# Kernel optimization log

Measured on AMD Instinct MI355X. Metric: run time of the kernel, lower is better.

Reference implementation:

```python
import jax, jax.numpy as jnp
import numpy as np

N, E, Q = 50000, 800000, 2000000   # nodes, edges, quadruplets
F_IN, H, OUT, G = 128, 128, 1, 64  # in_channels, hidden, out_channels, graphs
NRBF = NCBF = NSBF = 6
L = 3  # num_layers


def _mlp2(h, Wa, ba, Wb, bb):
    # Linear -> ReLU -> Linear
    return jax.nn.relu(h @ Wa + ba) @ Wb + bb


def setup_inputs() -> dict:
    key = jax.random.key(0)
    ks = jax.random.split(key, 24)
    s = 0.05
    inp = {
        "x": jax.random.normal(ks[0], (N, F_IN), jnp.float32),
        "rbf": jax.random.normal(ks[1], (E, NRBF), jnp.float32),
        "cbf": jax.random.normal(ks[2], (Q, NCBF), jnp.float32),
        "sbf": jax.random.normal(ks[3], (Q, NSBF), jnp.float32),
        "edge_index": jax.random.randint(ks[4], (2, E), 0, N),
        "l_idx": jax.random.randint(ks[5], (Q,), 0, N),
        "k_idx": jax.random.randint(ks[6], (Q,), 0, E),
        "batch": jnp.sort(jax.random.randint(ks[7], (N,), 0, G)),
        # per-layer params (all layers share shapes since F_IN == H)
        "W_e1a": s * jax.random.normal(ks[8], (L, F_IN + NRBF + NCBF + NSBF, H)),
        "b_e1a": jnp.zeros((L, H)),
        "W_e1b": s * jax.random.normal(ks[9], (L, H, H)),
        "b_e1b": jnp.zeros((L, H)),
        "W_e2a": s * jax.random.normal(ks[10], (L, 2 * H, H)),
        "b_e2a": jnp.zeros((L, H)),
        "W_e2b": s * jax.random.normal(ks[11], (L, H, H)),
        "b_e2b": jnp.zeros((L, H)),
        "W_na": s * jax.random.normal(ks[12], (L, F_IN + H, H)),
        "b_na": jnp.zeros((L, H)),
        "W_nb": s * jax.random.normal(ks[13], (L, H, H)),
        "b_nb": jnp.zeros((L, H)),
        "W_oa": s * jax.random.normal(ks[14], (H, H)),
        "b_oa": jnp.zeros((H,)),
        "W_ob": s * jax.random.normal(ks[15], (H, OUT)),
        "b_ob": jnp.zeros((OUT,)),
    }
    return inp


def reference(x, rbf, cbf, sbf,
              W_e1a, b_e1a, W_e1b, b_e1b,
              W_e2a, b_e2a, W_e2b, b_e2b,
              W_na, b_na, W_nb, b_nb,
              W_oa, b_oa, W_ob, b_ob,
              edge_index, l_idx, k_idx, batch):
    src, dst = edge_index[0], edge_index[1]  # x_j = x[src], index = dst
    h = x
    for p in range(L):
        # quadruplet message: gather-concat-MLP  [Q, F+18] -> [Q, H]
        m_in = jnp.concatenate([h[l_idx], rbf[k_idx], cbf, sbf], axis=-1)
        em = _mlp2(m_in, W_e1a[p], b_e1a[p], W_e1b[p], b_e1b[p])
        # scatter-add quadruplet messages onto edges by k_idx -> [E, H]
        agg_e = jax.ops.segment_sum(em, k_idx, num_segments=E)
        # second stage: per-edge concat (note: aggregated indexed by dst, as in source)
        fin = jnp.concatenate([h[src], agg_e[dst]], axis=-1)
        msg = _mlp2(fin, W_e2a[p], b_e2a[p], W_e2b[p], b_e2b[p])
        # aggregate edge messages to target nodes -> [N, H]
        aggr = jax.ops.segment_sum(msg, dst, num_segments=N)
        h = _mlp2(jnp.concatenate([h, aggr], axis=-1), W_na[p], b_na[p], W_nb[p], b_nb[p])
    # global mean pool over graphs
    counts = jax.ops.segment_sum(jnp.ones((N, 1), h.dtype), batch, num_segments=G)
    pooled = jax.ops.segment_sum(h, batch, num_segments=G) / jnp.maximum(counts, 1.0)
    pooled = jax.nn.relu(pooled)
    return _mlp2(pooled, W_oa, b_oa, W_ob, b_ob)
```

## Files before the change

### kernel.cpp

```cpp
#include <hip/hip_runtime.h>

constexpr int Nn = 50000;
constexpr int Ee = 800000;
constexpr int Qq = 2000000;
constexpr int Gg = 64;
constexpr int Hh = 128;
constexpr int NB64 = (Nn + 63) / 64;
constexpr int NSCB = (Nn + 1023) / 1024;

typedef short bf16x8 __attribute__((ext_vector_type(8)));
typedef float f32x4  __attribute__((ext_vector_type(4)));

__device__ __forceinline__ unsigned short f2bf(float f) {
    unsigned u = __builtin_bit_cast(unsigned, f);
    u += 0x7FFFu + ((u >> 16) & 1u);
    return (unsigned short)(u >> 16);
}
__device__ __forceinline__ float bf2f(unsigned short s) {
    unsigned u = ((unsigned)s) << 16;
    return __builtin_bit_cast(float, u);
}

__global__ void k_hist2(const int* __restrict__ dst, const int* __restrict__ kidx,
                        int* __restrict__ hist_e, int* __restrict__ hist_q) {
    int i = blockIdx.x * blockDim.x + threadIdx.x;
    if (i < Ee) atomicAdd(&hist_e[dst[i]], 1);
    if (i < Qq) { int v = kidx[i]; if (v < Nn) atomicAdd(&hist_q[v], 1); }
}

__global__ __launch_bounds__(1024) void k_scanA2(const int* __restrict__ he,
                                                 const int* __restrict__ hq,
                                                 int* __restrict__ ce, int* __restrict__ cq,
                                                 int* __restrict__ bs) {
    __shared__ int s[1024];
    const int* h = blockIdx.y ? hq : he;
    int* c = blockIdx.y ? cq : ce;
    int* b = bs + blockIdx.y * 64;
    const int tid = threadIdx.x;
    int i = blockIdx.x * 1024 + tid;
    int v = (i < Nn) ? h[i] : 0;
    s[tid] = v;
    __syncthreads();
    for (int off = 1; off < 1024; off <<= 1) {
        int t = (tid >= off) ? s[tid - off] : 0;
        __syncthreads();
        s[tid] += t;
        __syncthreads();
    }
    if (i < Nn) c[i] = s[tid] - v;
    if (tid == 1023) b[blockIdx.x] = s[1023];
}
__global__ void k_scanB2(int* __restrict__ bs) {
    __shared__ int s[64];
    int* b = bs + blockIdx.x * 64;
    const int tid = threadIdx.x;
    int v = (tid < NSCB) ? b[tid] : 0;
    s[tid] = v;
    __syncthreads();
    for (int off = 1; off < 64; off <<= 1) {
        int t = (tid >= off) ? s[tid - off] : 0;
        __syncthreads();
        s[tid] += t;
        __syncthreads();
    }
    if (tid < NSCB) b[tid] = s[tid] - v;
}
__global__ __launch_bounds__(1024) void k_scanC2(int* __restrict__ ce, int* __restrict__ cq,
                                                 const int* __restrict__ bs) {
    int* c = blockIdx.y ? cq : ce;
    const int* b = bs + blockIdx.y * 64;
    int i = blockIdx.x * 1024 + threadIdx.x;
    if (i < Nn) c[i] += b[blockIdx.x];
}

__global__ void k_scatter_both(const int* __restrict__ dst, const int* __restrict__ src,
                               const int* __restrict__ kidx, const int* __restrict__ lidx,
                               const float* __restrict__ cbf, const float* __restrict__ sbf,
                               int* __restrict__ cur_e, int* __restrict__ cur_q,
                               int* __restrict__ srcs, int* __restrict__ lq,
                               unsigned short* __restrict__ qfeat) {
    int i = blockIdx.x * blockDim.x + threadIdx.x;
    if (i < Ee) {
        int p = atomicAdd(&cur_e[dst[i]], 1);
        srcs[p] = src[i];
    }
    if (i < Qq) {
        int v = kidx[i];
        if (v < Nn) {
            int p = atomicAdd(&cur_q[v], 1);
            lq[p] = lidx[i];
            unsigned short f[12];
#pragma unroll
            for (int k = 0; k < 6; ++k) f[k] = f2bf(cbf[(size_t)i * 6 + k]);
#pragma unroll
            for (int k = 0; k < 6; ++k) f[6 + k] = f2bf(sbf[(size_t)i * 6 + k]);
            *(uint2*)&qfeat[(size_t)p * 12]     = *(uint2*)&f[0];
            *(uint2*)&qfeat[(size_t)p * 12 + 4] = *(uint2*)&f[4];
            *(uint2*)&qfeat[(size_t)p * 12 + 8] = *(uint2*)&f[8];
        }
    }
}

__global__ void k_wtall(const float* __restrict__ We1a0, const float* __restrict__ We1b0,
                        const float* __restrict__ We2a0, const float* __restrict__ We2b0,
                        const float* __restrict__ Wna0,  const float* __restrict__ Wnb0,
                        unsigned short* __restrict__ wbuf) {
    int idx = blockIdx.x * blockDim.x + threadIdx.x;
    if (idx >= 135168) return;
    const int p = blockIdx.y;
    const float* We1a = We1a0 + (size_t)p * 146 * 128;
    const float* We1b = We1b0 + (size_t)p * 128 * 128;
    const float* We2a = We2a0 + (size_t)p * 256 * 128;
    const float* We2b = We2b0 + (size_t)p * 128 * 128;
    const float* Wna  = Wna0  + (size_t)p * 256 * 128;
    const float* Wnb  = Wnb0  + (size_t)p * 128 * 128;
    unsigned short* base = wbuf + (size_t)p * 135168;
    const float* src; int K, Kp, loc;
    if (idx < 16384)       { src = We1a;             K = 128; Kp = 128; loc = idx; }
    else if (idx < 20480)  { src = We1a + 128 * 128; K = 6;   Kp = 32;  loc = idx - 16384; }
    else if (idx < 36864)  { src = We1b;             K = 128; Kp = 128; loc = idx - 20480; }
    else if (idx < 69632)  { src = We2a;             K = 256; Kp = 256; loc = idx - 36864; }
    else if (idx < 86016)  { src = We2b;             K = 128; Kp = 128; loc = idx - 69632; }
    else if (idx < 118784) { src = Wna;              K = 256; Kp = 256; loc = idx - 86016; }
    else                   { src = Wnb;              K = 128; Kp = 128; loc = idx - 118784; }
    int n = loc / Kp, k = loc - n * Kp;
    base[idx] = (k < K) ? f2bf(src[(size_t)k * 128 + n]) : (unsigned short)0;
}

__device__ __forceinline__ void zacc(f32x4 acc[4][2]) {
#pragma unroll
    for (int rt = 0; rt < 4; ++rt)
#pragma unroll
        for (int ct = 0; ct < 2; ++ct)
            acc[rt][ct] = (f32x4){0.f, 0.f, 0.f, 0.f};
}

template<int KK, int SA, int KP>
__device__ __forceinline__ void gemm64(const unsigned short* A,
                                       const unsigned short* __restrict__ Wt,
                                       int k_off, f32x4 acc[4][2]) {
    const int tid = threadIdx.x;
    const int lane = tid & 63;
    const int nb = (tid >> 6) * 32;
    const int rA = lane & 15;
    const int kg = lane >> 4;
#pragma unroll
    for (int ks = 0; ks < KK / 32; ++ks) {
        const int ka = ks * 32 + kg * 8;
        const int kb = k_off + ka;
        bf16x8 b0 = *(const bf16x8*)&Wt[(size_t)(nb + rA) * KP + kb];
        bf16x8 b1 = *(const bf16x8*)&Wt[(size_t)(nb + 16 + rA) * KP + kb];
#pragma unroll
        for (int rt = 0; rt < 4; ++rt) {
            bf16x8 a = *(const bf16x8*)&A[(rt * 16 + rA) * SA + ka];
            acc[rt][0] = __builtin_amdgcn_mfma_f32_16x16x32_bf16(a, b0, acc[rt][0], 0, 0, 0);
            acc[rt][1] = __builtin_amdgcn_mfma_f32_16x16x32_bf16(a, b1, acc[rt][1], 0, 0, 0);
        }
    }
}

__device__ __forceinline__ void store_acc(const f32x4 acc[4][2], unsigned short* out,
                                          int n0, int nmax) {
    const int tid = threadIdx.x;
    const int lane = tid & 63;
    const int nb = (tid >> 6) * 32;
    const int rA = lane & 15, kg = lane >> 4;
#pragma unroll
    for (int rt = 0; rt < 4; ++rt)
#pragma unroll
        for (int ct = 0; ct < 2; ++ct) {
            int col = nb + ct * 16 + rA;
#pragma unroll
            for (int i = 0; i < 4; ++i) {
                int n = n0 + rt * 16 + kg * 4 + i;
                if (n < nmax) out[(size_t)n * 128 + col] = f2bf(acc[rt][ct][i]);
            }
        }
}

__global__ __launch_bounds__(256) void k_pre0(
    const float* __restrict__ x, const float* __restrict__ rbf,
    const unsigned short* __restrict__ wbuf,
    unsigned short* __restrict__ hb,
    unsigned short* __restrict__ P1, unsigned short* __restrict__ Z1,
    unsigned short* __restrict__ P2all)
{
    __shared__ unsigned short TA[64 * 136];
    const int m0 = blockIdx.x * 64;
    const int tid = threadIdx.x;
    for (int i = tid; i < 64 * 32; i += 256) {
        int row = i >> 5, c = i & 31;
        int n = m0 + row;
        int nc = min(n, Nn - 1);
        float4 v = *(const float4*)&x[(size_t)nc * 128 + c * 4];
        ushort4 o;
        o.x = f2bf(v.x); o.y = f2bf(v.y); o.z = f2bf(v.z); o.w = f2bf(v.w);
        *(ushort4*)&TA[row * 136 + c * 4] = o;
        if (n < Nn) *(ushort4*)&hb[(size_t)n * 128 + c * 4] = o;
    }
    __syncthreads();
    f32x4 acc[4][2];
    zacc(acc);
    gemm64<128, 136, 128>(TA, wbuf, 0, acc);
    store_acc(acc, P1, m0, Nn);
    zacc(acc);
    gemm64<128, 136, 256>(TA, wbuf + 36864, 0, acc);
    store_acc(acc, Z1, m0, Nn);
    __syncthreads();
    for (int i = tid; i < 64 * 32; i += 256) {
        int row = i >> 5, c = i & 31;
        int nc = min(m0 + row, Nn - 1);
        float v = (c < 6) ? rbf[(size_t)nc * 6 + c] : 0.f;
        TA[row * 136 + c] = f2bf(v);
    }
    __syncthreads();
    for (int p = 0; p < 3; ++p) {
        zacc(acc);
        gemm64<32, 136, 32>(TA, wbuf + (size_t)p * 135168 + 16384, 0, acc);
        store_acc(acc, P2all + (size_t)p * Nn * 128, m0, Nn);
    }
}

__global__ __launch_bounds__(256) void k_quadagg(
    const unsigned short* __restrict__ P1, const unsigned short* __restrict__ P2,
    const unsigned short* __restrict__ qfeat, const int* __restrict__ lq,
    const int* __restrict__ rowend, const int* __restrict__ rowcnt,
    const float* __restrict__ We1a_raw, const float* __restrict__ b_e1a,
    unsigned short* __restrict__ Rb)
{
    __shared__ float W34[12 * 128];
    __shared__ float bia[128];
    const int tid = threadIdx.x;
    for (int i = tid; i < 12 * 128; i += 256) W34[i] = We1a_raw[134 * 128 + i];
    if (tid < 128) bia[tid] = b_e1a[tid];
    __syncthreads();
    const int nd = tid >> 4;
    const int c0 = (tid & 15) * 8;
    const int n = blockIdx.x * 16 + nd;
    const int end = rowend[n];
    const int beg = end - rowcnt[n];
    float base[8];
    {
        uint4 p2v = *(const uint4*)&P2[(size_t)n * 128 + c0];
        const unsigned short* pp = (const unsigned short*)&p2v;
#pragma unroll
        for (int k = 0; k < 8; ++k) base[k] = bia[c0 + k] + bf2f(pp[k]);
    }
    float acc[8];
#pragma unroll
    for (int k = 0; k < 8; ++k) acc[k] = 0.f;
    for (int e = beg; e < end; ++e) {
        int l = lq[e];
        uint4 a = *(const uint4*)&P1[(size_t)l * 128 + c0];
        uint2 f0 = *(const uint2*)&qfeat[(size_t)e * 12];
        uint2 f1 = *(const uint2*)&qfeat[(size_t)e * 12 + 4];
        uint2 f2 = *(const uint2*)&qfeat[(size_t)e * 12 + 8];
        const unsigned short* q0 = (const unsigned short*)&f0;
        const unsigned short* q1 = (const unsigned short*)&f1;
        const unsigned short* q2 = (const unsigned short*)&f2;
        float qv[12] = {bf2f(q0[0]), bf2f(q0[1]), bf2f(q0[2]), bf2f(q0[3]),
                        bf2f(q1[0]), bf2f(q1[1]), bf2f(q1[2]), bf2f(q1[3]),
                        bf2f(q2[0]), bf2f(q2[1]), bf2f(q2[2]), bf2f(q2[3])};
        const unsigned short* ap = (const unsigned short*)&a;
        float t[8];
#pragma unroll
        for (int k = 0; k < 8; ++k) t[k] = base[k] + bf2f(ap[k]);
#pragma unroll
        for (int kk = 0; kk < 12; ++kk) {
            float q_ = qv[kk];
#pragma unroll
            for (int k = 0; k < 8; ++k)
                t[k] = fmaf(q_, W34[kk * 128 + c0 + k], t[k]);
        }
#pragma unroll
        for (int k = 0; k < 8; ++k) acc[k] += fmaxf(t[k], 0.f);
    }
    unsigned short ov[8];
#pragma unroll
    for (int k = 0; k < 8; ++k) ov[k] = f2bf(acc[k]);
    *(uint4*)&Rb[(size_t)n * 128 + c0] = *(uint4*)ov;
}

__global__ __launch_bounds__(256) void k_edgeagg(
    const unsigned short* __restrict__ Z1, const unsigned short* __restrict__ Z2,
    const int* __restrict__ srcs,
    const int* __restrict__ rowend, const int* __restrict__ rowcnt,
    const float* __restrict__ b_e2a,
    unsigned short* __restrict__ Rb)
{
    const int tid = threadIdx.x;
    const int nd = tid >> 4;
    const int c0 = (tid & 15) * 8;
    const int n = blockIdx.x * 16 + nd;
    const int end = rowend[n];
    const int beg = end - rowcnt[n];
    float z2b[8];
    {
        uint4 zv = *(const uint4*)&Z2[(size_t)n * 128 + c0];
        const unsigned short* zp = (const unsigned short*)&zv;
        float4 b0 = *(const float4*)&b_e2a[c0];
        float4 b1 = *(const float4*)&b_e2a[c0 + 4];
        z2b[0] = b0.x + bf2f(zp[0]); z2b[1] = b0.y + bf2f(zp[1]);
        z2b[2] = b0.z + bf2f(zp[2]); z2b[3] = b0.w + bf2f(zp[3]);
        z2b[4] = b1.x + bf2f(zp[4]); z2b[5] = b1.y + bf2f(zp[5]);
        z2b[6] = b1.z + bf2f(zp[6]); z2b[7] = b1.w + bf2f(zp[7]);
    }
    float acc[8];
#pragma unroll
    for (int k = 0; k < 8; ++k) acc[k] = 0.f;
    int e = beg;
    for (; e + 2 <= end; e += 2) {
        int s0 = srcs[e], s1 = srcs[e + 1];
        uint4 a0 = *(const uint4*)&Z1[(size_t)s0 * 128 + c0];
        uint4 a1 = *(const uint4*)&Z1[(size_t)s1 * 128 + c0];
        const unsigned short* p0 = (const unsigned short*)&a0;
        const unsigned short* p1 = (const unsigned short*)&a1;
#pragma unroll
        for (int k = 0; k < 8; ++k) acc[k] += fmaxf(z2b[k] + bf2f(p0[k]), 0.f);
#pragma unroll
        for (int k = 0; k < 8; ++k) acc[k] += fmaxf(z2b[k] + bf2f(p1[k]), 0.f);
    }
    if (e < end) {
        int s0 = srcs[e];
        uint4 a0 = *(const uint4*)&Z1[(size_t)s0 * 128 + c0];
        const unsigned short* p0 = (const unsigned short*)&a0;
#pragma unroll
        for (int k = 0; k < 8; ++k) acc[k] += fmaxf(z2b[k] + bf2f(p0[k]), 0.f);
    }
    unsigned short ov[8];
#pragma unroll
    for (int k = 0; k < 8; ++k) ov[k] = f2bf(acc[k]);
    *(uint4*)&Rb[(size_t)n * 128 + c0] = *(uint4*)ov;
}

__global__ __launch_bounds__(256) void k_agg2z(
    const unsigned short* __restrict__ Rb, const int* __restrict__ cntq,
    const unsigned short* __restrict__ wb, const float* __restrict__ b_e1b,
    unsigned short* __restrict__ Z2)
{
    __shared__ unsigned short L[64 * 136];
    __shared__ int rc[64];
    const int m0 = blockIdx.x * 64;
    const int tid = threadIdx.x;
    const unsigned short* We1bt = wb + 20480;
    const unsigned short* We2at = wb + 36864;
    if (tid < 64) rc[tid] = (m0 + tid < Nn) ? cntq[m0 + tid] : 0;
    for (int i = tid; i < 64 * 16; i += 256) {
        int row = i >> 4, ch = i & 15;
        int n = min(m0 + row, Nn - 1);
        *(uint4*)&L[row * 136 + ch * 8] = *(const uint4*)&Rb[(size_t)n * 128 + ch * 8];
    }
    __syncthreads();
    f32x4 acc[4][2];
    zacc(acc);
    gemm64<128, 136, 128>(L, We1bt, 0, acc);
    __syncthreads();
    {
        const int lane = tid & 63;
        const int nb = (tid >> 6) * 32;
        const int rA = lane & 15, kg = lane >> 4;
#pragma unroll
        for (int rt = 0; rt < 4; ++rt)
#pragma unroll
            for (int ct = 0; ct < 2; ++ct) {
                int col = nb + ct * 16 + rA;
                float bias = b_e1b[col];
#pragma unroll
                for (int i = 0; i < 4; ++i) {
                    int row = rt * 16 + kg * 4 + i;
                    L[row * 136 + col] = f2bf(acc[rt][ct][i] + (float)rc[row] * bias);
                }
            }
    }
    __syncthreads();
    zacc(acc);
    gemm64<128, 136, 256>(L, We2at, 128, acc);
    store_acc(acc, Z2, m0, Nn);
}

template<int LAST>
__global__ __launch_bounds__(256) void k_nodeNew(
    const unsigned short* __restrict__ Rb, const int* __restrict__ deg,
    const unsigned short* __restrict__ wb,
    const float* __restrict__ b_e2b, const float* __restrict__ b_na,
    const float* __restrict__ b_nb,
    unsigned short* __restrict__ hb,
    const unsigned short* __restrict__ wbn,
    unsigned short* __restrict__ P1n, unsigned short* __restrict__ Z1n)
{
    __shared__ unsigned short L[64 * 136];
    __shared__ int rc[64];
    const int m0 = blockIdx.x * 64;
    const int tid = threadIdx.x;
    const unsigned short* We2bt = wb + 69632;
    const unsigned short* Wnat  = wb + 86016;
    const unsigned short* Wnbt  = wb + 118784;
    const int lane = tid & 63;
    const int nb = (tid >> 6) * 32;
    const int rA = lane & 15, kg = lane >> 4;
    if (tid < 64) rc[tid] = (m0 + tid < Nn) ? deg[m0 + tid] : 0;
    for (int i = tid; i < 64 * 16; i += 256) {
        int row = i >> 4, ch = i & 15;
        int n = min(m0 + row, Nn - 1);
        *(uint4*)&L[row * 136 + ch * 8] = *(const uint4*)&Rb[(size_t)n * 128 + ch * 8];
    }
    __syncthreads();
    f32x4 acc[4][2];
    zacc(acc);
    gemm64<128, 136, 128>(L, We2bt, 0, acc);
    __syncthreads();
#pragma unroll
    for (int rt = 0; rt < 4; ++rt)
#pragma unroll
        for (int ct = 0; ct < 2; ++ct) {
            int col = nb + ct * 16 + rA;
            float bias = b_e2b[col];
#pragma unroll
            for (int i = 0; i < 4; ++i) {
                int row = rt * 16 + kg * 4 + i;
                L[row * 136 + col] = f2bf(acc[rt][ct][i] + (float)rc[row] * bias);
            }
        }
    __syncthreads();
    f32x4 acc2[4][2];
    zacc(acc2);
    gemm64<128, 136, 256>(L, Wnat, 128, acc2);
    __syncthreads();
    for (int i = tid; i < 64 * 16; i += 256) {
        int row = i >> 4, ch = i & 15;
        int n = min(m0 + row, Nn - 1);
        *(uint4*)&L[row * 136 + ch * 8] = *(const uint4*)&hb[(size_t)n * 128 + ch * 8];
    }
    __syncthreads();
    gemm64<128, 136, 256>(L, Wnat, 0, acc2);
    __syncthreads();
#pragma unroll
    for (int rt = 0; rt < 4; ++rt)
#pragma unroll
        for (int ct = 0; ct < 2; ++ct) {
            int col = nb + ct * 16 + rA;
            float bias = b_na[col];
#pragma unroll
            for (int i = 0; i < 4; ++i) {
                int row = rt * 16 + kg * 4 + i;
                L[row * 136 + col] = f2bf(fmaxf(acc2[rt][ct][i] + bias, 0.f));
            }
        }
    __syncthreads();
    zacc(acc);
    gemm64<128, 136, 128>(L, Wnbt, 0, acc);
    __syncthreads();
#pragma unroll
    for (int rt = 0; rt < 4; ++rt)
#pragma unroll
        for (int ct = 0; ct < 2; ++ct) {
            int col = nb + ct * 16 + rA;
            float bias = b_nb[col];
#pragma unroll
            for (int i = 0; i < 4; ++i) {
                int row = rt * 16 + kg * 4 + i;
                int n = m0 + row;
                unsigned short hv = f2bf(acc[rt][ct][i] + bias);
                if (n < Nn) hb[(size_t)n * 128 + col] = hv;
                if (!LAST) L[row * 136 + col] = hv;
            }
        }
    if (!LAST) {
        __syncthreads();
        zacc(acc);
        gemm64<128, 136, 128>(L, wbn, 0, acc);
        store_acc(acc, P1n, m0, Nn);
        zacc(acc);
        gemm64<128, 136, 256>(L, wbn + 36864, 0, acc);
        store_acc(acc, Z1n, m0, Nn);
    }
}

__global__ __launch_bounds__(256) void k_pool(const unsigned short* __restrict__ hb,
                                              const int* __restrict__ batch,
                                              float* __restrict__ pooled,
                                              float* __restrict__ cntg) {
    __shared__ int bseg[200];
    constexpr int CH = 196;
    const int start = blockIdx.x * CH;
    const int end = min(start + CH, Nn);
    if (start >= end) return;
    const int tid = threadIdx.x;
    for (int i = tid; i < end - start; i += 256) bseg[i] = batch[start + i];
    __syncthreads();
    const int j = tid & 127;
    const int rh = tid >> 7;
    float acc = 0.f, cacc = 0.f;
    int cur = -1;
    for (int n = start + rh; n < end; n += 2) {
        int g = bseg[n - start];
        if (g != cur) {
            if (cur >= 0) {
                atomicAdd(&pooled[cur * Hh + j], acc);
                if (j == 0) atomicAdd(&cntg[cur], cacc);
            }
            cur = g; acc = 0.f; cacc = 0.f;
        }
        acc += bf2f(hb[(size_t)n * Hh + j]);
        cacc += 1.f;
    }
    if (cur >= 0) {
        atomicAdd(&pooled[cur * Hh + j], acc);
        if (j == 0) atomicAdd(&cntg[cur], cacc);
    }
}

__global__ __launch_bounds__(128) void k_final(
    const float* __restrict__ pooled, const float* __restrict__ cntg,
    const float* __restrict__ Woa, const float* __restrict__ boa,
    const float* __restrict__ Wob, const float* __restrict__ bob,
    float* __restrict__ out)
{
    __shared__ float p[128];
    __shared__ float t[128];
    __shared__ float red[128];
    const int g = blockIdx.x;
    const int j = threadIdx.x;
    float c = fmaxf(cntg[g], 1.f);
    p[j] = fmaxf(pooled[g * Hh + j] / c, 0.f);
    __syncthreads();
    float acc = boa[j];
    for (int d = 0; d < Hh; ++d) acc = fmaf(p[d], Woa[d * Hh + j], acc);
    t[j] = fmaxf(acc, 0.f);
    __syncthreads();
    red[j] = t[j] * Wob[j];
    __syncthreads();
    for (int s = 64; s > 0; s >>= 1) {
        if (j < s) red[j] += red[j + s];
        __syncthreads();
    }
    if (j == 0) out[g] = red[0] + bob[0];
}

extern "C" void kernel_launch(void* const* d_in, const int* in_sizes, int n_in,
                              void* d_out, int out_size, void* d_ws, size_t ws_size,
                              hipStream_t stream) {
    const float* x     = (const float*)d_in[0];
    const float* rbf   = (const float*)d_in[1];
    const float* cbf   = (const float*)d_in[2];
    const float* sbf   = (const float*)d_in[3];
    const int*   eidx  = (const int*)d_in[4];
    const int*   l_idx = (const int*)d_in[5];
    const int*   k_idx = (const int*)d_in[6];
    const int*   batch = (const int*)d_in[7];
    const float* W_e1a = (const float*)d_in[8];
    const float* b_e1a = (const float*)d_in[9];
    const float* W_e1b = (const float*)d_in[10];
    const float* b_e1b = (const float*)d_in[11];
    const float* W_e2a = (const float*)d_in[12];
    const float* b_e2a = (const float*)d_in[13];
    const float* W_e2b = (const float*)d_in[14];
    const float* b_e2b = (const float*)d_in[15];
    const float* W_na  = (const float*)d_in[16];
    const float* b_na  = (const float*)d_in[17];
    const float* W_nb  = (const float*)d_in[18];
    const float* b_nb  = (const float*)d_in[19];
    const float* W_oa  = (const float*)d_in[20];
    const float* b_oa  = (const float*)d_in[21];
    const float* W_ob  = (const float*)d_in[22];
    const float* b_ob  = (const float*)d_in[23];

    const int* src = eidx;
    const int* dst = eidx + Ee;

    const size_t NHb = (size_t)Nn * Hh * sizeof(unsigned short);
    char* w = (char*)d_ws;
    unsigned short* hb   = (unsigned short*)w; w += NHb;
    unsigned short* P1a  = (unsigned short*)w; w += NHb;
    unsigned short* P1b  = (unsigned short*)w; w += NHb;
    unsigned short* Z1a  = (unsigned short*)w; w += NHb;
    unsigned short* Z1b  = (unsigned short*)w; w += NHb;
    unsigned short* Z2   = (unsigned short*)w; w += NHb;
    unsigned short* Rb   = (unsigned short*)w; w += NHb;
    unsigned short* P2all = (unsigned short*)w; w += 3 * NHb;
    float* pooled = (float*)w; w += (size_t)Gg * Hh * sizeof(float);
    float* cntg   = (float*)w; w += (size_t)Gg * sizeof(float);
    int*   lq     = (int*)w;   w += (size_t)Qq * sizeof(int);
    unsigned short* qfeat = (unsigned short*)w; w += (size_t)Qq * 12 * sizeof(unsigned short);
    int*   srcs_e = (int*)w;   w += (size_t)Ee * sizeof(int);
    int*   hist_e = (int*)w;   w += (size_t)Nn * sizeof(int);
    int*   hist_q = (int*)w;   w += (size_t)Nn * sizeof(int);
    int*   cur_e  = (int*)w;   w += (size_t)Nn * sizeof(int);
    int*   cur_q  = (int*)w;   w += (size_t)Nn * sizeof(int);
    int*   bsum   = (int*)w;   w += 128 * sizeof(int);
    unsigned short* wbuf = (unsigned short*)w;

    const size_t LSTRIDE = 135168;

    hipMemsetAsync(hist_e, 0, 2 * Nn * sizeof(int), stream);
    k_hist2<<<(Qq + 255) / 256, 256, 0, stream>>>(dst, k_idx, hist_e, hist_q);
    {
        dim3 g(NSCB, 2);
        k_scanA2<<<g, 1024, 0, stream>>>(hist_e, hist_q, cur_e, cur_q, bsum);
        k_scanB2<<<2, 64, 0, stream>>>(bsum);
        k_scanC2<<<g, 1024, 0, stream>>>(cur_e, cur_q, bsum);
    }
    k_scatter_both<<<(Qq + 255) / 256, 256, 0, stream>>>(dst, src, k_idx, l_idx,
        cbf, sbf, cur_e, cur_q, srcs_e, lq, qfeat);

    {
        dim3 g((135168 + 255) / 256, 3);
        k_wtall<<<g, 256, 0, stream>>>(W_e1a, W_e1b, W_e2a, W_e2b, W_na, W_nb, wbuf);
    }
    k_pre0<<<NB64, 256, 0, stream>>>(x, rbf, wbuf, hb, P1a, Z1a, P2all);

    unsigned short* P1s[2] = { P1a, P1b };
    unsigned short* Z1s[2] = { Z1a, Z1b };
    for (int p = 0; p < 3; ++p) {
        const unsigned short* wb = wbuf + p * LSTRIDE;
        const unsigned short* wbn = wbuf + ((p + 1) % 3) * LSTRIDE;
        int c = p & 1;
        k_quadagg<<<Nn / 16, 256, 0, stream>>>(P1s[c],
            P2all + (size_t)p * Nn * 128, qfeat, lq, cur_q, hist_q,
            W_e1a + (size_t)p * 146 * 128, b_e1a + (size_t)p * 128, Rb);
        k_agg2z<<<NB64, 256, 0, stream>>>(Rb, hist_q, wb, b_e1b + (size_t)p * 128, Z2);
        k_edgeagg<<<Nn / 16, 256, 0, stream>>>(Z1s[c], Z2, srcs_e, cur_e, hist_e,
            b_e2a + (size_t)p * 128, Rb);
        if (p < 2)
            k_nodeNew<0><<<NB64, 256, 0, stream>>>(Rb, hist_e, wb,
                b_e2b + (size_t)p * 128, b_na + (size_t)p * 128, b_nb + (size_t)p * 128,
                hb, wbn, P1s[c ^ 1], Z1s[c ^ 1]);
        else
            k_nodeNew<1><<<NB64, 256, 0, stream>>>(Rb, hist_e, wb,
                b_e2b + (size_t)p * 128, b_na + (size_t)p * 128, b_nb + (size_t)p * 128,
                hb, wbn, P1s[c ^ 1], Z1s[c ^ 1]);
    }
    hipMemsetAsync(pooled, 0, (size_t)(Gg * Hh + Gg) * sizeof(float), stream);
    k_pool<<<(Nn + 195) / 196, 256, 0, stream>>>(hb, batch, pooled, cntg);
    k_final<<<Gg, 128, 0, stream>>>(pooled, cntg, W_oa, b_oa, W_ob, b_ob, (float*)d_out);
}
```

Before: 533.6 us.

## Sort nodes by degree for balanced aggregation and pack quad records

Result: slower. 876.5 us (+64.3%).

```diff
diff --git a/kernel.cpp b/kernel.cpp
--- a/kernel.cpp
+++ b/kernel.cpp
@@ -77,8 +77,7 @@
                                const int* __restrict__ kidx, const int* __restrict__ lidx,
                                const float* __restrict__ cbf, const float* __restrict__ sbf,
                                int* __restrict__ cur_e, int* __restrict__ cur_q,
-                               int* __restrict__ srcs, int* __restrict__ lq,
-                               unsigned short* __restrict__ qfeat) {
+                               int* __restrict__ srcs, unsigned short* __restrict__ qrec) {
     int i = blockIdx.x * blockDim.x + threadIdx.x;
     if (i < Ee) {
         int p = atomicAdd(&cur_e[dst[i]], 1);
@@ -88,17 +87,63 @@
         int v = kidx[i];
         if (v < Nn) {
             int p = atomicAdd(&cur_q[v], 1);
-            lq[p] = lidx[i];
-            unsigned short f[12];
-#pragma unroll
-            for (int k = 0; k < 6; ++k) f[k] = f2bf(cbf[(size_t)i * 6 + k]);
-#pragma unroll
-            for (int k = 0; k < 6; ++k) f[6 + k] = f2bf(sbf[(size_t)i * 6 + k]);
-            *(uint2*)&qfeat[(size_t)p * 12]     = *(uint2*)&f[0];
-            *(uint2*)&qfeat[(size_t)p * 12 + 4] = *(uint2*)&f[4];
-            *(uint2*)&qfeat[(size_t)p * 12 + 8] = *(uint2*)&f[8];
-        }
-    }
+            unsigned short rec[16];
+            ((int*)rec)[0] = lidx[i];
+#pragma unroll
+            for (int k = 0; k < 6; ++k) rec[2 + k] = f2bf(cbf[(size_t)i * 6 + k]);
+#pragma unroll
+            for (int k = 0; k < 6; ++k) rec[8 + k] = f2bf(sbf[(size_t)i * 6 + k]);
+            rec[14] = 0; rec[15] = 0;
+            *(uint4*)&qrec[(size_t)p * 16]     = *(uint4*)&rec[0];
+            *(uint4*)&qrec[(size_t)p * 16 + 8] = *(uint4*)&rec[8];
+        }
+    }
+}
+
+__global__ void k_histdeg(const int* __restrict__ he, const int* __restrict__ hq,
+                          int* __restrict__ dbins) {
+    __shared__ int lh[512];
+    const int tid = threadIdx.x;
+    for (int i = tid; i < 512; i += 256) lh[i] = 0;
+    __syncthreads();
+    int i = blockIdx.x * 256 + tid;
+    if (i < Nn) {
+        atomicAdd(&lh[min(he[i], 255)], 1);
+        atomicAdd(&lh[256 + min(hq[i], 255)], 1);
+    }
+    __syncthreads();
+    for (int j = tid; j < 512; j += 256) {
+        int v = lh[j];
+        if (v) atomicAdd(&dbins[j], v);
+    }
+}
+__global__ __launch_bounds__(256) void k_scandeg(const int* __restrict__ dbins,
+                                                 int* __restrict__ dcur) {
+    __shared__ int s[256];
+    const int tid = threadIdx.x;
+    for (int sec = 0; sec < 2; ++sec) {
+        int v = dbins[sec * 256 + tid];
+        s[tid] = v;
+        __syncthreads();
+        for (int off = 1; off < 256; off <<= 1) {
+            int t = (tid >= off) ? s[tid - off] : 0;
+            __syncthreads();
+            s[tid] += t;
+            __syncthreads();
+        }
+        dcur[sec * 256 + tid] = s[tid] - v;
+        __syncthreads();
+    }
+}
+__global__ void k_scatterdeg(const int* __restrict__ he, const int* __restrict__ hq,
+                             int* __restrict__ dcur,
+                             int* __restrict__ order_e, int* __restrict__ order_q) {
+    int i = blockIdx.x * blockDim.x + threadIdx.x;
+    if (i >= Nn) return;
+    int pe = atomicAdd(&dcur[min(he[i], 255)], 1);
+    order_e[pe] = i;
+    int pq = atomicAdd(&dcur[256 + min(hq[i], 255)], 1);
+    order_q[pq] = i;
 }
 
 __global__ void k_wtall(const float* __restrict__ We1a0, const float* __restrict__ We1b0,
@@ -223,8 +268,9 @@
 
 __global__ __launch_bounds__(256) void k_quadagg(
     const unsigned short* __restrict__ P1, const unsigned short* __restrict__ P2,
-    const unsigned short* __restrict__ qfeat, const int* __restrict__ lq,
+    const unsigned short* __restrict__ qrec,
     const int* __restrict__ rowend, const int* __restrict__ rowcnt,
+    const int* __restrict__ order,
     const float* __restrict__ We1a_raw, const float* __restrict__ b_e1a,
     unsigned short* __restrict__ Rb)
 {
@@ -236,7 +282,7 @@
     __syncthreads();
     const int nd = tid >> 4;
     const int c0 = (tid & 15) * 8;
-    const int n = blockIdx.x * 16 + nd;
+    const int n = order[blockIdx.x * 16 + nd];
     const int end = rowend[n];
     const int beg = end - rowcnt[n];
     float base[8];
@@ -250,17 +296,15 @@
 #pragma unroll
     for (int k = 0; k < 8; ++k) acc[k] = 0.f;
     for (int e = beg; e < end; ++e) {
-        int l = lq[e];
+        uint4 r0 = *(const uint4*)&qrec[(size_t)e * 16];
+        uint4 r1 = *(const uint4*)&qrec[(size_t)e * 16 + 8];
+        int l = ((const int*)&r0)[0];
         uint4 a = *(const uint4*)&P1[(size_t)l * 128 + c0];
-        uint2 f0 = *(const uint2*)&qfeat[(size_t)e * 12];
-        uint2 f1 = *(const uint2*)&qfeat[(size_t)e * 12 + 4];
-        uint2 f2 = *(const uint2*)&qfeat[(size_t)e * 12 + 8];
-        const unsigned short* q0 = (const unsigned short*)&f0;
-        const unsigned short* q1 = (const unsigned short*)&f1;
-        const unsigned short* q2 = (const unsigned short*)&f2;
-        float qv[12] = {bf2f(q0[0]), bf2f(q0[1]), bf2f(q0[2]), bf2f(q0[3]),
-                        bf2f(q1[0]), bf2f(q1[1]), bf2f(q1[2]), bf2f(q1[3]),
-                        bf2f(q2[0]), bf2f(q2[1]), bf2f(q2[2]), bf2f(q2[3])};
+        const unsigned short* q0 = (const unsigned short*)&r0;
+        const unsigned short* q1 = (const unsigned short*)&r1;
+        float qv[12] = {bf2f(q0[2]), bf2f(q0[3]), bf2f(q0[4]), bf2f(q0[5]),
+                        bf2f(q0[6]), bf2f(q0[7]), bf2f(q1[0]), bf2f(q1[1]),
+                        bf2f(q1[2]), bf2f(q1[3]), bf2f(q1[4]), bf2f(q1[5])};
         const unsigned short* ap = (const unsigned short*)&a;
         float t[8];
 #pragma unroll
@@ -285,13 +329,14 @@
     const unsigned short* __restrict__ Z1, const unsigned short* __restrict__ Z2,
     const int* __restrict__ srcs,
     const int* __restrict__ rowend, const int* __restrict__ rowcnt,
+    const int* __restrict__ order,
     const float* __restrict__ b_e2a,
     unsigned short* __restrict__ Rb)
 {
     const int tid = threadIdx.x;
     const int nd = tid >> 4;
     const int c0 = (tid & 15) * 8;
-    const int n = blockIdx.x * 16 + nd;
+    const int n = order[blockIdx.x * 16 + nd];
     const int end = rowend[n];
     const int beg = end - rowcnt[n];
     float z2b[8];
@@ -309,6 +354,25 @@
 #pragma unroll
     for (int k = 0; k < 8; ++k) acc[k] = 0.f;
     int e = beg;
+    for (; e + 4 <= end; e += 4) {
+        int s0 = srcs[e], s1 = srcs[e + 1], s2 = srcs[e + 2], s3 = srcs[e + 3];
+        uint4 a0 = *(const uint4*)&Z1[(size_t)s0 * 128 + c0];
+        uint4 a1 = *(const uint4*)&Z1[(size_t)s1 * 128 + c0];
+        uint4 a2 = *(const uint4*)&Z1[(size_t)s2 * 128 + c0];
+        uint4 a3 = *(const uint4*)&Z1[(size_t)s3 * 128 + c0];
+        const unsigned short* p0 = (const unsigned short*)&a0;
+        const unsigned short* p1 = (const unsigned short*)&a1;
+        const unsigned short* p2 = (const unsigned short*)&a2;
+        const unsigned short* p3 = (const unsigned short*)&a3;
+#pragma unroll
+        for (int k = 0; k < 8; ++k) acc[k] += fmaxf(z2b[k] + bf2f(p0[k]), 0.f);
+#pragma unroll
+        for (int k = 0; k < 8; ++k) acc[k] += fmaxf(z2b[k] + bf2f(p1[k]), 0.f);
+#pragma unroll
+        for (int k = 0; k < 8; ++k) acc[k] += fmaxf(z2b[k] + bf2f(p2[k]), 0.f);
+#pragma unroll
+        for (int k = 0; k < 8; ++k) acc[k] += fmaxf(z2b[k] + bf2f(p3[k]), 0.f);
+    }
     for (; e + 2 <= end; e += 2) {
         int s0 = srcs[e], s1 = srcs[e + 1];
         uint4 a0 = *(const uint4*)&Z1[(size_t)s0 * 128 + c0];
@@ -580,19 +644,22 @@
     unsigned short* P2all = (unsigned short*)w; w += 3 * NHb;
     float* pooled = (float*)w; w += (size_t)Gg * Hh * sizeof(float);
     float* cntg   = (float*)w; w += (size_t)Gg * sizeof(float);
-    int*   lq     = (int*)w;   w += (size_t)Qq * sizeof(int);
-    unsigned short* qfeat = (unsigned short*)w; w += (size_t)Qq * 12 * sizeof(unsigned short);
+    unsigned short* qrec = (unsigned short*)w; w += (size_t)Qq * 16 * sizeof(unsigned short);
     int*   srcs_e = (int*)w;   w += (size_t)Ee * sizeof(int);
     int*   hist_e = (int*)w;   w += (size_t)Nn * sizeof(int);
     int*   hist_q = (int*)w;   w += (size_t)Nn * sizeof(int);
+    int*   dbins  = (int*)w;   w += 512 * sizeof(int);
+    int*   dcur   = (int*)w;   w += 512 * sizeof(int);
     int*   cur_e  = (int*)w;   w += (size_t)Nn * sizeof(int);
     int*   cur_q  = (int*)w;   w += (size_t)Nn * sizeof(int);
     int*   bsum   = (int*)w;   w += 128 * sizeof(int);
+    int*   order_e = (int*)w;  w += (size_t)Nn * sizeof(int);
+    int*   order_q = (int*)w;  w += (size_t)Nn * sizeof(int);
     unsigned short* wbuf = (unsigned short*)w;
 
     const size_t LSTRIDE = 135168;
 
-    hipMemsetAsync(hist_e, 0, 2 * Nn * sizeof(int), stream);
+    hipMemsetAsync(hist_e, 0, (2 * (size_t)Nn + 1024) * sizeof(int), stream);
     k_hist2<<<(Qq + 255) / 256, 256, 0, stream>>>(dst, k_idx, hist_e, hist_q);
     {
         dim3 g(NSCB, 2);
@@ -601,7 +668,11 @@
         k_scanC2<<<g, 1024, 0, stream>>>(cur_e, cur_q, bsum);
     }
     k_scatter_both<<<(Qq + 255) / 256, 256, 0, stream>>>(dst, src, k_idx, l_idx,
-        cbf, sbf, cur_e, cur_q, srcs_e, lq, qfeat);
+        cbf, sbf, cur_e, cur_q, srcs_e, qrec);
+    k_histdeg<<<(Nn + 255) / 256, 256, 0, stream>>>(hist_e, hist_q, dbins);
+    k_scandeg<<<1, 256, 0, stream>>>(dbins, dcur);
+    k_scatterdeg<<<(Nn + 255) / 256, 256, 0, stream>>>(hist_e, hist_q, dcur,
+        order_e, order_q);
 
     {
         dim3 g((135168 + 255) / 256, 3);
@@ -616,11 +687,11 @@
         const unsigned short* wbn = wbuf + ((p + 1) % 3) * LSTRIDE;
         int c = p & 1;
         k_quadagg<<<Nn / 16, 256, 0, stream>>>(P1s[c],
-            P2all + (size_t)p * Nn * 128, qfeat, lq, cur_q, hist_q,
+            P2all + (size_t)p * Nn * 128, qrec, cur_q, hist_q, order_q,
             W_e1a + (size_t)p * 146 * 128, b_e1a + (size_t)p * 128, Rb);
         k_agg2z<<<NB64, 256, 0, stream>>>(Rb, hist_q, wb, b_e1b + (size_t)p * 128, Z2);
         k_edgeagg<<<Nn / 16, 256, 0, stream>>>(Z1s[c], Z2, srcs_e, cur_e, hist_e,
-            b_e2a + (size_t)p * 128, Rb);
+            order_e, b_e2a + (size_t)p * 128, Rb);
         if (p < 2)
             k_nodeNew<0><<<NB64, 256, 0, stream>>>(Rb, hist_e, wb,
                 b_e2b + (size_t)p * 128, b_na + (size_t)p * 128, b_nb + (size_t)p * 128,
```
